# Performance work log

Measured on AMD Instinct MI355X. Metric: run time of the kernel, lower is better.

## Reference

```python
import jax, jax.numpy as jnp
import numpy as np

D_MODEL = 1024
N_HEAD = 16
D_HEAD = D_MODEL // N_HEAD
N_CTX = 2048
ROPE_BASE = 10000.0
SCALE = 1


def _rope_cache(seq_len, d_head, dtype=jnp.float32):
    inv_freq = 1.0 / (ROPE_BASE ** (jnp.arange(0, d_head, 2, dtype=jnp.float32) / d_head))
    t = jnp.arange(seq_len, dtype=jnp.float32)
    freqs = jnp.outer(t, inv_freq)              # [S, d_head/2]
    emb = jnp.concatenate([freqs, freqs], -1)   # [S, d_head]  (concat, per source)
    cos = jnp.cos(emb)[None, :, None, :].astype(dtype)
    sin = jnp.sin(emb)[None, :, None, :].astype(dtype)
    return cos, sin


def _apply_rope(x, cos, sin):
    # x: [B, S, H, Dh]; interleaved rotate (stack then flatten), per source
    x_even = x[..., 0::2]
    x_odd = x[..., 1::2]
    x_rot = jnp.stack([-x_odd, x_even], axis=-1).reshape(x.shape)
    return x * cos + x_rot * sin


def _rmsnorm(x, w):
    eps = jnp.finfo(x.dtype).eps  # torch RMSNorm default eps
    var = jnp.mean(jnp.square(x), axis=-1, keepdims=True)
    return x * jax.lax.rsqrt(var + eps) * w


def setup_inputs() -> dict:
    key = jax.random.key(0)
    ks = jax.random.split(key, 9)
    B, S = 2, N_CTX
    x = jax.random.normal(ks[0], (B, S, D_MODEL), jnp.float32)
    s = 0.02
    Wq = jax.random.normal(ks[1], (D_MODEL, D_MODEL), jnp.float32) * s
    bq = jax.random.normal(ks[2], (D_MODEL,), jnp.float32) * s
    Wk = jax.random.normal(ks[3], (D_MODEL, D_MODEL), jnp.float32) * s
    bk = jax.random.normal(ks[4], (D_MODEL,), jnp.float32) * s
    Wv = jax.random.normal(ks[5], (D_MODEL, D_MODEL), jnp.float32) * s
    bv = jax.random.normal(ks[6], (D_MODEL,), jnp.float32) * s
    Wo = jax.random.normal(ks[7], (D_MODEL, D_MODEL), jnp.float32) * s
    norm_w = jnp.ones((D_HEAD,), jnp.float32)
    return {"x": x, "Wq": Wq, "bq": bq, "Wk": Wk, "bk": bk,
            "Wv": Wv, "bv": bv, "Wo": Wo, "norm_w": norm_w}


def reference(x, Wq, bq, Wk, bk, Wv, bv, Wo, norm_w):
    B, S, _ = x.shape
    split = lambda t: t.reshape(B, S, N_HEAD, D_HEAD)
    q = split(x @ Wq.T + bq)
    k = split(x @ Wk.T + bk)
    v = split(x @ Wv.T + bv)
    cos, sin = _rope_cache(S, D_HEAD, x.dtype)
    q = _apply_rope(_rmsnorm(q, norm_w), cos, sin)
    k = _apply_rope(_rmsnorm(k, norm_w), cos, sin)
    scores = jnp.einsum('bqhd,bkhd->bhqk', q, k)
    causal = jnp.tril(jnp.ones((S, S), x.dtype))
    pattern = jnp.square(scores / D_HEAD) * causal  # quadratic score, masked
    z = jnp.einsum('bhqk,bkhd->bqhd', pattern, v).reshape(B, S, D_MODEL)
    return x + (z @ Wo.T) * SCALE
```

## Files before the change

### kernel.cpp

```cpp
#include <hip/hip_runtime.h>
#include <math.h>


typedef float  f32x4  __attribute__((ext_vector_type(4)));
typedef short  bf16x8 __attribute__((ext_vector_type(8)));
typedef float  vf4    __attribute__((ext_vector_type(4)));
typedef unsigned short u16x4 __attribute__((ext_vector_type(4)));

static __device__ __forceinline__ unsigned short f2bf(float f) {
    union { float f; unsigned int i; } c; c.f = f;
    unsigned int x = c.i;
    return (unsigned short)((x + 0x7fffu + ((x >> 16) & 1u)) >> 16);
}
static __device__ __forceinline__ f32x4 shfl_xor4(f32x4 v, int m) {
    f32x4 r;
    r[0] = __shfl_xor(v[0], m); r[1] = __shfl_xor(v[1], m);
    r[2] = __shfl_xor(v[2], m); r[3] = __shfl_xor(v[3], m);
    return r;
}
static __device__ __forceinline__ f32x4 rsq4(f32x4 v) {
    f32x4 r;
#pragma unroll
    for (int i = 0; i < 4; i++) r[i] = rsqrtf(v[i] * (1.0f / 64.0f) + 1.1920929e-07f);
    return r;
}
static __device__ __forceinline__ void cp16(const unsigned short* g, unsigned short* l) {
    __builtin_amdgcn_global_load_lds(
        (const __attribute__((address_space(1))) unsigned int*)g,
        (__attribute__((address_space(3))) unsigned int*)l, 16, 0, 0);
}

#define FOR_2(X)  X(0) X(1)
#define FOR_M(X)  X(0) X(1) X(2) X(3)
#define FOR_MN(X) X(0,0) X(0,1) X(0,2) X(0,3) X(1,0) X(1,1) X(1,2) X(1,3) \
                  X(2,0) X(2,1) X(2,2) X(2,3) X(3,0) X(3,1) X(3,2) X(3,3)
#define FOR_MN2(X) X(0,0) X(0,1) X(0,2) X(0,3) X(1,0) X(1,1) X(1,2) X(1,3)

#define MF(c,a,b) c = __builtin_amdgcn_mfma_f32_16x16x32_bf16(a, b, c, 0, 0, 0);

__global__ __launch_bounds__(256) void cvt_all(
    const float* __restrict__ x,  const float* __restrict__ Wq,
    const float* __restrict__ Wk, const float* __restrict__ Wv,
    const float* __restrict__ Wo,
    unsigned short* __restrict__ xb,  unsigned short* __restrict__ Wqb,
    unsigned short* __restrict__ Wkb, unsigned short* __restrict__ Wvb,
    unsigned short* __restrict__ Wob, int nx4, int nw4)
{
    int i = blockIdx.x * 256 + threadIdx.x;
    const float* s; unsigned short* d; int li;
    if (i < nx4) { s = x; d = xb; li = i; }
    else {
        int idx = i - nx4;
        int r = idx / nw4; li = idx - r * nw4;
        if (r >= 4) return;
        s = (r == 0) ? Wq : (r == 1) ? Wk : (r == 2) ? Wv : Wo;
        d = (r == 0) ? Wqb : (r == 1) ? Wkb : (r == 2) ? Wvb : Wob;
    }
    vf4 v = *(const vf4*)(s + (size_t)li * 4);
    u16x4 o;
#pragma unroll
    for (int j = 0; j < 4; j++) o[j] = f2bf(v[j]);
    *(u16x4*)(d + (size_t)li * 4) = o;
}

#define SS 136

__global__ __launch_bounds__(256, 3) void gemm_qkvz(
    const unsigned short* __restrict__ xb,
    const unsigned short* __restrict__ Wqb,
    const unsigned short* __restrict__ Wkb,
    const unsigned short* __restrict__ Wvb,
    const float* __restrict__ bqf, const float* __restrict__ bkf, const float* __restrict__ bvf,
    const float* __restrict__ nwp,
    unsigned short* __restrict__ qb, unsigned short* __restrict__ kb,
    unsigned short* __restrict__ vT)
{
    const int K = 1024;
    __shared__ unsigned short smem[24576];
    const int z = blockIdx.z;
    const unsigned short* Wb = (z == 0) ? Wqb : (z == 1) ? Wkb : Wvb;
    const float* bias = (z == 0) ? bqf : (z == 1) ? bkf : bvf;
    const int tid = threadIdx.x;
    const int n0 = blockIdx.x * 128;
    const int m0 = blockIdx.y * 128;
    const int lane = tid & 63, wid = tid >> 6;
    const int wy = wid >> 1, wx = wid & 1;
    const int l15 = lane & 15, quad = lane >> 4;
    const int r16 = lane >> 2;
    const int c8  = (lane & 3) * 8;

#define Z_DECL_ACC(mi,ni) f32x4 c##mi##ni = {0.f, 0.f, 0.f, 0.f};
    FOR_MN(Z_DECL_ACC)

#define Z_STAGE(BUF, KT) { \
        unsigned short* dstb = smem + (BUF) * 8192; \
        _Pragma("unroll") \
        for (int j = 0; j < 4; j++) { \
            const int ch = wid * 4 + j;           \
            const int mat = ch >> 3;              \
            const int row = (ch & 7) * 16 + r16; \
            const unsigned short* g = mat \
                ? Wb + (size_t)(n0 + row) * K + (KT) + c8 \
                : xb + (size_t)(m0 + row) * K + (KT) + c8; \
            cp16(g, &dstb[ch * 512]); \
        } }

#define Z_COMPUTE(BUF) { \
        const unsigned short* As_ = smem + (BUF) * 8192; \
        const unsigned short* Bs_ = As_ + 4096; \
        const bf16x8 a0 = *(const bf16x8*)&As_[(wy * 64 +  0 + l15) * 32 + quad * 8]; \
        const bf16x8 a1 = *(const bf16x8*)&As_[(wy * 64 + 16 + l15) * 32 + quad * 8]; \
        const bf16x8 a2 = *(const bf16x8*)&As_[(wy * 64 + 32 + l15) * 32 + quad * 8]; \
        const bf16x8 a3 = *(const bf16x8*)&As_[(wy * 64 + 48 + l15) * 32 + quad * 8]; \
        const bf16x8 b0 = *(const bf16x8*)&Bs_[(wx * 64 +  0 + l15) * 32 + quad * 8]; \
        const bf16x8 b1 = *(const bf16x8*)&Bs_[(wx * 64 + 16 + l15) * 32 + quad * 8]; \
        const bf16x8 b2 = *(const bf16x8*)&Bs_[(wx * 64 + 32 + l15) * 32 + quad * 8]; \
        const bf16x8 b3 = *(const bf16x8*)&Bs_[(wx * 64 + 48 + l15) * 32 + quad * 8]; \
        MF(c00,a0,b0) MF(c01,a0,b1) MF(c02,a0,b2) MF(c03,a0,b3) \
        MF(c10,a1,b0) MF(c11,a1,b1) MF(c12,a1,b2) MF(c13,a1,b3) \
        MF(c20,a2,b0) MF(c21,a2,b1) MF(c22,a2,b2) MF(c23,a2,b3) \
        MF(c30,a3,b0) MF(c31,a3,b1) MF(c32,a3,b2) MF(c33,a3,b3) }

    Z_STAGE(0, 0)
    Z_STAGE(1, 32)
    {
        int cbuf = 0, sbuf = 2;
        for (int it = 0; it < 31; ++it) {
            asm volatile("s_waitcnt vmcnt(4)" ::: "memory");
            __builtin_amdgcn_s_barrier();
            if (it < 30) { Z_STAGE(sbuf, (it + 2) * 32) }
            Z_COMPUTE(cbuf)
            asm volatile("s_waitcnt lgkmcnt(0)" ::: "memory");
            cbuf = (cbuf == 2) ? 0 : cbuf + 1;
            sbuf = (sbuf == 2) ? 0 : sbuf + 1;
        }
        asm volatile("s_waitcnt vmcnt(0)" ::: "memory");
        __builtin_amdgcn_s_barrier();
        Z_COMPUTE(cbuf)
    }
    __syncthreads();

    const float bs0 = bias[n0 + wx * 64 + l15];
    const float bs1 = bias[n0 + wx * 64 + 16 + l15];
    const float bs2 = bias[n0 + wx * 64 + 32 + l15];
    const float bs3 = bias[n0 + wx * 64 + 48 + l15];
#define Z_BIAS(mi) c##mi##0 += bs0; c##mi##1 += bs1; c##mi##2 += bs2; c##mi##3 += bs3;
    FOR_M(Z_BIAS)

    if (z < 2) {
        const float nww0 = nwp[l15],      nww1 = nwp[16 + l15];
        const float nww2 = nwp[32 + l15], nww3 = nwp[48 + l15];
        const float lf0 = expf(-(float)l15 * 0.28782313662425572f);
        const float lf1 = expf(-(float)(l15 + 16) * 0.28782313662425572f);

#define Z_S2(mi) f32x4 s2_##mi = c##mi##0*c##mi##0 + c##mi##1*c##mi##1 + \
                                 c##mi##2*c##mi##2 + c##mi##3*c##mi##3; \
        s2_##mi = s2_##mi + shfl_xor4(s2_##mi, 1); \
        s2_##mi = s2_##mi + shfl_xor4(s2_##mi, 2); \
        s2_##mi = s2_##mi + shfl_xor4(s2_##mi, 4); \
        s2_##mi = s2_##mi + shfl_xor4(s2_##mi, 8); \
        s2_##mi = rsq4(s2_##mi);
        FOR_M(Z_S2)

#define Z_ROPE_ONE(mi,ni,NW,CS,SN) { \
            float vn = c##mi##ni[r] * s2v[r] * NW; \
            float pt = __shfl_xor(vn, 1); \
            float rot = (lane & 1) ? pt : -pt; \
            smem[mrow * SS + wx * 64 + (ni) * 16 + l15] = f2bf((vn * (CS) + rot * (SN)) * 0.125f); }
#define Z_ROPE_MI(mi) { f32x4 s2v = s2_##mi; \
            _Pragma("unroll") \
            for (int r = 0; r < 4; r++) { \
                const int mrow = wy * 64 + (mi) * 16 + quad * 4 + r; \
                const float t = (float)((m0 + mrow) & 2047); \
                const float a0 = t * lf0, a1 = t * lf1; \
                const float cs0 = cosf(a0), sn0 = sinf(a0); \
                const float cs1 = cosf(a1), sn1 = sinf(a1); \
                Z_ROPE_ONE(mi,0,nww0,cs0,sn0) Z_ROPE_ONE(mi,1,nww1,cs1,sn1) \
                Z_ROPE_ONE(mi,2,nww2,cs0,sn0) Z_ROPE_ONE(mi,3,nww3,cs1,sn1) } }
        FOR_M(Z_ROPE_MI)

        __syncthreads();
        unsigned short* dst = z ? kb : qb;
#pragma unroll
        for (int it = 0; it < 8; it++) {
            const int linear = tid + it * 256;
            const int row = linear >> 4, cb = linear & 15;
            *(bf16x8*)(dst + (size_t)(m0 + row) * 1024 + n0 + cb * 8) =
                *(const bf16x8*)&smem[row * SS + cb * 8];
        }
    } else {
#define Z_VST(mi,ni) { _Pragma("unroll") \
            for (int r = 0; r < 4; r++) { \
                const int mrow = wy * 64 + (mi) * 16 + quad * 4 + r; \
                smem[(wx * 64 + (ni) * 16 + l15) * SS + mrow] = f2bf(c##mi##ni[r]); } }
        FOR_MN(Z_VST)
        __syncthreads();
        const int b = m0 >> 11, tok0 = m0 & 2047;
#pragma unroll
        for (int it = 0; it < 8; it++) {
            const int linear = tid + it * 256;
            const int rowd = linear >> 4, cb = linear & 15;
            const int head_g = (n0 >> 6) + (rowd >> 6);
            const int d = rowd & 63;
            *(bf16x8*)(vT + (((size_t)b * 16 + head_g) * 64 + d) * 2048 + tok0 + cb * 8) =
                *(const bf16x8*)&smem[rowd * SS + cb * 8];
        }
    }
}

__global__ __launch_bounds__(512) void gemm_out(
    const unsigned short* __restrict__ zb,
    const unsigned short* __restrict__ Wob,
    const float* __restrict__ x, float* __restrict__ out, int M)
{
    const int K = 1024;
    __shared__ unsigned short smem[24576];
    const int tid = threadIdx.x;
    const int n0 = blockIdx.x * 128;
    const int m0 = blockIdx.y * 128;
    const int lane = tid & 63, wid = tid >> 6;
    const int wy = wid >> 1, wx = wid & 1;
    const int l15 = lane & 15, quad = lane >> 4;
    const int r16 = lane >> 2;
    const int c8  = (lane & 3) * 8;

#define G_DECL_ACC(mi,ni) f32x4 c##mi##ni = {0.f, 0.f, 0.f, 0.f};
    FOR_MN2(G_DECL_ACC)

#define O_STAGE(BUF, KT) { \
        unsigned short* dstb = smem + (BUF) * 8192; \
        _Pragma("unroll") \
        for (int j = 0; j < 2; j++) { \
            const int ch = wid * 2 + j;           \
            const int mat = ch >> 3;              \
            const int row = (ch & 7) * 16 + r16; \
            const unsigned short* g = (mat == 0) \
                ? zb  + (size_t)(m0 + row) * K + (KT) + c8 \
                : Wob + (size_t)(n0 + row) * K + (KT) + c8; \
            cp16(g, &dstb[ch * 512]); \
        } }

#define O_COMPUTE(BUF) { \
        const unsigned short* As_ = smem + (BUF) * 8192; \
        const unsigned short* Ws_ = As_ + 4096; \
        const bf16x8 a0 = *(const bf16x8*)&As_[(wy * 32 +  0 + l15) * 32 + quad * 8]; \
        const bf16x8 a1 = *(const bf16x8*)&As_[(wy * 32 + 16 + l15) * 32 + quad * 8]; \
        const bf16x8 b0 = *(const bf16x8*)&Ws_[(wx * 64 +  0 + l15) * 32 + quad * 8]; \
        const bf16x8 b1 = *(const bf16x8*)&Ws_[(wx * 64 + 16 + l15) * 32 + quad * 8]; \
        const bf16x8 b2 = *(const bf16x8*)&Ws_[(wx * 64 + 32 + l15) * 32 + quad * 8]; \
        const bf16x8 b3 = *(const bf16x8*)&Ws_[(wx * 64 + 48 + l15) * 32 + quad * 8]; \
        MF(c00,a0,b0) MF(c01,a0,b1) MF(c02,a0,b2) MF(c03,a0,b3) \
        MF(c10,a1,b0) MF(c11,a1,b1) MF(c12,a1,b2) MF(c13,a1,b3) }

    O_STAGE(0, 0)
    O_STAGE(1, 32)
    {
        int cbuf = 0, sbuf = 2;
        for (int it = 0; it < 31; ++it) {
            asm volatile("s_waitcnt vmcnt(2)" ::: "memory");
            __builtin_amdgcn_s_barrier();
            if (it < 30) { O_STAGE(sbuf, (it + 2) * 32) }
            O_COMPUTE(cbuf)
            asm volatile("s_waitcnt lgkmcnt(0)" ::: "memory");
            cbuf = (cbuf == 2) ? 0 : cbuf + 1;
            sbuf = (sbuf == 2) ? 0 : sbuf + 1;
        }
        asm volatile("s_waitcnt vmcnt(0)" ::: "memory");
        __builtin_amdgcn_s_barrier();
        O_COMPUTE(cbuf)
    }

#define G_OUTST(mi,ni) { _Pragma("unroll") \
        for (int r = 0; r < 4; r++) { \
            const int m = m0 + wy * 32 + (mi) * 16 + quad * 4 + r; \
            const int n = n0 + wx * 64 + (ni) * 16 + l15; \
            out[(size_t)m * 1024 + n] = c##mi##ni[r] + x[(size_t)m * 1024 + n]; } }
    FOR_MN2(G_OUTST)
}

__global__ __launch_bounds__(256) void attn_mfma(
    const unsigned short* __restrict__ qb, const unsigned short* __restrict__ kb,
    const unsigned short* __restrict__ vT, unsigned short* __restrict__ zb)
{
    __shared__ unsigned short Qs[128 * 72];
    __shared__ unsigned short Ks[64 * 72];
    __shared__ unsigned short Vs[64 * 72];
    __shared__ unsigned short Pm[128 * 72];
    const int tid = threadIdx.x;

    const int bid = blockIdx.x;
    const int halfsz = gridDim.x >> 1;
    const int half = (bid >= halfsz) ? 1 : 0;
    const int r = bid - half * halfsz;
    const int qt = half ? (r & 7) : 15 - (r & 7);
    const int bh = r >> 3;

    const int b = bh >> 4, h = bh & 15;
    const int lane = tid & 63, wq = tid >> 6;
    const int l15 = lane & 15, quad = lane >> 4;
    const size_t tokbase = (size_t)b * 2048;
    const int q0 = qt * 128;

#pragma unroll
    for (int j = 0; j < 4; j++) {
        const int u = tid + j * 256;
        const int row = u >> 3, seg = (u & 7) * 8;
        bf16x8 v = *(const bf16x8*)(qb + (tokbase + q0 + row) * 1024 + h * 64 + seg);
        *(bf16x8*)&Qs[row * 72 + seg] = v;
    }
    __syncthreads();
    const bf16x8 aq00 = *(const bf16x8*)&Qs[(wq * 32 + l15) * 72 + quad * 8];
    const bf16x8 aq01 = *(const bf16x8*)&Qs[(wq * 32 + l15) * 72 + 32 + quad * 8];
    const bf16x8 aq10 = *(const bf16x8*)&Qs[(wq * 32 + 16 + l15) * 72 + quad * 8];
    const bf16x8 aq11 = *(const bf16x8*)&Qs[(wq * 32 + 16 + l15) * 72 + 32 + quad * 8];

    const int kr = tid >> 3;
    const int sg = (tid & 7) * 8;

    bf16x8 pk0, pk1, pv0, pv1;
#define A_GLB(KT) { \
        pk0 = *(const bf16x8*)(kb + (tokbase + (KT) * 64 + kr) * 1024 + h * 64 + sg); \
        pk1 = *(const bf16x8*)(kb + (tokbase + (KT) * 64 + kr + 32) * 1024 + h * 64 + sg); \
        pv0 = *(const bf16x8*)(vT + ((size_t)bh * 64 + kr) * 2048 + (KT) * 64 + sg); \
        pv1 = *(const bf16x8*)(vT + ((size_t)bh * 64 + kr + 32) * 2048 + (KT) * 64 + sg); }

#define A_DECL_Z(mi,n) f32x4 z_##mi##n = {0.f, 0.f, 0.f, 0.f};
    FOR_MN2(A_DECL_Z)

    const int nkt = 2 * qt + 2;
    A_GLB(0)
    for (int kt = 0; kt < nkt; kt++) {
        __syncthreads();
        *(bf16x8*)&Ks[kr * 72 + sg] = pk0;
        *(bf16x8*)&Ks[(kr + 32) * 72 + sg] = pk1;
        *(bf16x8*)&Vs[kr * 72 + sg] = pv0;
        *(bf16x8*)&Vs[(kr + 32) * 72 + sg] = pv1;
        __syncthreads();
        if (kt + 1 < nkt) A_GLB(kt + 1)

#define A_DECL_S(mi,n) f32x4 s_##mi##n = {0.f, 0.f, 0.f, 0.f};
        FOR_MN2(A_DECL_S)
#define A_QKH(KS, AQ0, AQ1) { \
        bf16x8 b0 = *(const bf16x8*)&Ks[(l15) * 72 + (KS) * 32 + quad * 8]; \
        bf16x8 b1 = *(const bf16x8*)&Ks[(16 + l15) * 72 + (KS) * 32 + quad * 8]; \
        bf16x8 b2 = *(const bf16x8*)&Ks[(32 + l15) * 72 + (KS) * 32 + quad * 8]; \
        bf16x8 b3 = *(const bf16x8*)&Ks[(48 + l15) * 72 + (KS) * 32 + quad * 8]; \
        s_00 = __builtin_amdgcn_mfma_f32_16x16x32_bf16(AQ0, b0, s_00, 0, 0, 0); \
        s_01 = __builtin_amdgcn_mfma_f32_16x16x32_bf16(AQ0, b1, s_01, 0, 0, 0); \
        s_02 = __builtin_amdgcn_mfma_f32_16x16x32_bf16(AQ0, b2, s_02, 0, 0, 0); \
        s_03 = __builtin_amdgcn_mfma_f32_16x16x32_bf16(AQ0, b3, s_03, 0, 0, 0); \
        s_10 = __builtin_amdgcn_mfma_f32_16x16x32_bf16(AQ1, b0, s_10, 0, 0, 0); \
        s_11 = __builtin_amdgcn_mfma_f32_16x16x32_bf16(AQ1, b1, s_11, 0, 0, 0); \
        s_12 = __builtin_amdgcn_mfma_f32_16x16x32_bf16(AQ1, b2, s_12, 0, 0, 0); \
        s_13 = __builtin_amdgcn_mfma_f32_16x16x32_bf16(AQ1, b3, s_13, 0, 0, 0); }
        A_QKH(0, aq00, aq10)
        A_QKH(1, aq01, aq11)

        const bool needmask = (kt >= 2 * qt);
#define A_PSTORE(mi,n) { \
        f32x4 p4 = s_##mi##n * s_##mi##n; \
        if (needmask) { _Pragma("unroll") \
            for (int r2 = 0; r2 < 4; r2++) \
                if (kt * 64 + (n) * 16 + l15 > q0 + wq * 32 + (mi) * 16 + quad * 4 + r2) p4[r2] = 0.f; } \
        _Pragma("unroll") \
        for (int r2 = 0; r2 < 4; r2++) \
            Pm[(wq * 32 + (mi) * 16 + quad * 4 + r2) * 72 + (n) * 16 + l15] = f2bf(p4[r2]); }
        FOR_MN2(A_PSTORE)

#define A_PVH(KS) { \
        bf16x8 ap0 = *(const bf16x8*)&Pm[(wq * 32 + l15) * 72 + (KS) * 32 + quad * 8]; \
        bf16x8 ap1 = *(const bf16x8*)&Pm[(wq * 32 + 16 + l15) * 72 + (KS) * 32 + quad * 8]; \
        bf16x8 u0 = *(const bf16x8*)&Vs[(l15) * 72 + (KS) * 32 + quad * 8]; \
        bf16x8 u1 = *(const bf16x8*)&Vs[(16 + l15) * 72 + (KS) * 32 + quad * 8]; \
        bf16x8 u2 = *(const bf16x8*)&Vs[(32 + l15) * 72 + (KS) * 32 + quad * 8]; \
        bf16x8 u3 = *(const bf16x8*)&Vs[(48 + l15) * 72 + (KS) * 32 + quad * 8]; \
        z_00 = __builtin_amdgcn_mfma_f32_16x16x32_bf16(ap0, u0, z_00, 0, 0, 0); \
        z_01 = __builtin_amdgcn_mfma_f32_16x16x32_bf16(ap0, u1, z_01, 0, 0, 0); \
        z_02 = __builtin_amdgcn_mfma_f32_16x16x32_bf16(ap0, u2, z_02, 0, 0, 0); \
        z_03 = __builtin_amdgcn_mfma_f32_16x16x32_bf16(ap0, u3, z_03, 0, 0, 0); \
        z_10 = __builtin_amdgcn_mfma_f32_16x16x32_bf16(ap1, u0, z_10, 0, 0, 0); \
        z_11 = __builtin_amdgcn_mfma_f32_16x16x32_bf16(ap1, u1, z_11, 0, 0, 0); \
        z_12 = __builtin_amdgcn_mfma_f32_16x16x32_bf16(ap1, u2, z_12, 0, 0, 0); \
        z_13 = __builtin_amdgcn_mfma_f32_16x16x32_bf16(ap1, u3, z_13, 0, 0, 0); }
        A_PVH(0)
        A_PVH(1)
    }

#define A_ZST(mi,n) { _Pragma("unroll") \
        for (int r2 = 0; r2 < 4; r2++) \
            Pm[(wq * 32 + (mi) * 16 + quad * 4 + r2) * 72 + (n) * 16 + l15] = f2bf(z_##mi##n[r2]); }
    FOR_MN2(A_ZST)
#pragma unroll
    for (int it = 0; it < 4; it++) {
        const int linear = it * 64 + lane;
        const int row = linear >> 3, cb = linear & 7;
        *(bf16x8*)(zb + (tokbase + q0 + wq * 32 + row) * 1024 + h * 64 + cb * 8) =
            *(const bf16x8*)&Pm[(wq * 32 + row) * 72 + cb * 8];
    }
}

extern "C" void kernel_launch(void* const* d_in, const int* in_sizes, int n_in,
                              void* d_out, int out_size, void* d_ws, size_t ws_size,
                              hipStream_t stream)
{
    const float* x  = (const float*)d_in[0];
    const float* Wq = (const float*)d_in[1];
    const float* bq = (const float*)d_in[2];
    const float* Wk = (const float*)d_in[3];
    const float* bk = (const float*)d_in[4];
    const float* Wv = (const float*)d_in[5];
    const float* bv = (const float*)d_in[6];
    const float* Wo = (const float*)d_in[7];
    const float* nw = (const float*)d_in[8];
    float* out = (float*)d_out;

    const int D = 1024;
    const int M = in_sizes[0] / D;

    unsigned short* xbb = (unsigned short*)d_ws;
    unsigned short* Wqb = xbb + (size_t)M * D;
    unsigned short* Wkb = Wqb + (size_t)D * D;
    unsigned short* Wvb = Wkb + (size_t)D * D;
    unsigned short* Wob = Wvb + (size_t)D * D;
    unsigned short* qbw = Wob + (size_t)D * D;
    unsigned short* kbw = qbw + (size_t)M * D;
    unsigned short* vTw = kbw + (size_t)M * D;
    unsigned short* zbw = vTw + (size_t)M * D;

    const int nx4 = M * D / 4, nw4 = D * D / 4;
    const int ncvt = nx4 + 4 * nw4;
    cvt_all<<<(ncvt + 255) / 256, 256, 0, stream>>>(
        x, Wq, Wk, Wv, Wo, xbb, Wqb, Wkb, Wvb, Wob, nx4, nw4);

    gemm_qkvz<<<dim3(D / 128, M / 128, 3), 256, 0, stream>>>(
        xbb, Wqb, Wkb, Wvb, bq, bk, bv, nw, qbw, kbw, vTw);

    attn_mfma<<<dim3((M / 2048) * 16 * 16), 256, 0, stream>>>(qbw, kbw, vTw, zbw);

    gemm_out<<<dim3(D / 128, M / 128), 512, 0, stream>>>(zbw, Wob, x, out, M);
}
```

Baseline: 197.2 us.

## Enlarge QKV GEMM tile to 256x256 with XOR-swizzled LDS and BK=64

Restructures the fused QKV projection GEMM to use 256x256 output tiles per 512-thread block with 8 waves, each computing a 128x64 sub-tile. K-step grows to 64 with an XOR-swizzled LDS layout to avoid bank conflicts, and the pipeline becomes double-buffered. Epilogue staging through shared memory is split into two halves to fit the buffer. The aim is more data reuse per global load and fewer blocks, at the cost of fewer blocks (96) than CUs, more registers and 128KB of LDS per block.

```diff
diff --git a/kernel.cpp b/kernel.cpp
--- a/kernel.cpp
+++ b/kernel.cpp
@@ -30,11 +30,13 @@
         (__attribute__((address_space(3))) unsigned int*)l, 16, 0, 0);
 }
 
-#define FOR_2(X)  X(0) X(1)
 #define FOR_M(X)  X(0) X(1) X(2) X(3)
-#define FOR_MN(X) X(0,0) X(0,1) X(0,2) X(0,3) X(1,0) X(1,1) X(1,2) X(1,3) \
-                  X(2,0) X(2,1) X(2,2) X(2,3) X(3,0) X(3,1) X(3,2) X(3,3)
+#define FOR_M8(X) X(0) X(1) X(2) X(3) X(4) X(5) X(6) X(7)
 #define FOR_MN2(X) X(0,0) X(0,1) X(0,2) X(0,3) X(1,0) X(1,1) X(1,2) X(1,3)
+#define FOR_MN84(X) X(0,0) X(0,1) X(0,2) X(0,3) X(1,0) X(1,1) X(1,2) X(1,3) \
+                    X(2,0) X(2,1) X(2,2) X(2,3) X(3,0) X(3,1) X(3,2) X(3,3) \
+                    X(4,0) X(4,1) X(4,2) X(4,3) X(5,0) X(5,1) X(5,2) X(5,3) \
+                    X(6,0) X(6,1) X(6,2) X(6,3) X(7,0) X(7,1) X(7,2) X(7,3)
 
 #define MF(c,a,b) c = __builtin_amdgcn_mfma_f32_16x16x32_bf16(a, b, c, 0, 0, 0);
 
@@ -63,9 +65,9 @@
     *(u16x4*)(d + (size_t)li * 4) = o;
 }
 
-#define SS 136
-
-__global__ __launch_bounds__(256, 3) void gemm_qkvz(
+#define SS2 264
+
+__global__ __launch_bounds__(512, 2) void gemm_qkvz(
     const unsigned short* __restrict__ xb,
     const unsigned short* __restrict__ Wqb,
     const unsigned short* __restrict__ Wkb,
@@ -76,68 +78,73 @@
     unsigned short* __restrict__ vT)
 {
     const int K = 1024;
-    __shared__ unsigned short smem[24576];
+    __shared__ unsigned short smem[65536];
     const int z = blockIdx.z;
     const unsigned short* Wb = (z == 0) ? Wqb : (z == 1) ? Wkb : Wvb;
     const float* bias = (z == 0) ? bqf : (z == 1) ? bkf : bvf;
     const int tid = threadIdx.x;
-    const int n0 = blockIdx.x * 128;
-    const int m0 = blockIdx.y * 128;
+    const int n0 = blockIdx.x * 256;
+    const int m0 = blockIdx.y * 256;
     const int lane = tid & 63, wid = tid >> 6;
-    const int wy = wid >> 1, wx = wid & 1;
+    const int wy = wid >> 2, wx = wid & 3;
     const int l15 = lane & 15, quad = lane >> 4;
-    const int r16 = lane >> 2;
-    const int c8  = (lane & 3) * 8;
+    const int sw = (l15 & 7) << 4;
+    const int srow = tid >> 3;
+    const int sc16 = tid & 7;
 
 #define Z_DECL_ACC(mi,ni) f32x4 c##mi##ni = {0.f, 0.f, 0.f, 0.f};
-    FOR_MN(Z_DECL_ACC)
-
-#define Z_STAGE(BUF, KT) { \
-        unsigned short* dstb = smem + (BUF) * 8192; \
+    FOR_MN84(Z_DECL_ACC)
+
+#define ZSTAGE(BUF, KT) { \
+        unsigned short* dstb = smem + (BUF) * 32768; \
         _Pragma("unroll") \
         for (int j = 0; j < 4; j++) { \
-            const int ch = wid * 4 + j;           \
-            const int mat = ch >> 3;              \
-            const int row = (ch & 7) * 16 + r16; \
-            const unsigned short* g = mat \
-                ? Wb + (size_t)(n0 + row) * K + (KT) + c8 \
-                : xb + (size_t)(m0 + row) * K + (KT) + c8; \
-            cp16(g, &dstb[ch * 512]); \
+            const int row = j * 64 + srow; \
+            const int gc = sc16 ^ (row & 7); \
+            cp16(xb + (size_t)(m0 + row) * K + (KT) + gc * 8, \
+                 dstb + row * 64 + sc16 * 8); \
+            cp16(Wb + (size_t)(n0 + row) * K + (KT) + gc * 8, \
+                 dstb + 16384 + row * 64 + sc16 * 8); \
         } }
 
-#define Z_COMPUTE(BUF) { \
-        const unsigned short* As_ = smem + (BUF) * 8192; \
-        const unsigned short* Bs_ = As_ + 4096; \
-        const bf16x8 a0 = *(const bf16x8*)&As_[(wy * 64 +  0 + l15) * 32 + quad * 8]; \
-        const bf16x8 a1 = *(const bf16x8*)&As_[(wy * 64 + 16 + l15) * 32 + quad * 8]; \
-        const bf16x8 a2 = *(const bf16x8*)&As_[(wy * 64 + 32 + l15) * 32 + quad * 8]; \
-        const bf16x8 a3 = *(const bf16x8*)&As_[(wy * 64 + 48 + l15) * 32 + quad * 8]; \
-        const bf16x8 b0 = *(const bf16x8*)&Bs_[(wx * 64 +  0 + l15) * 32 + quad * 8]; \
-        const bf16x8 b1 = *(const bf16x8*)&Bs_[(wx * 64 + 16 + l15) * 32 + quad * 8]; \
-        const bf16x8 b2 = *(const bf16x8*)&Bs_[(wx * 64 + 32 + l15) * 32 + quad * 8]; \
-        const bf16x8 b3 = *(const bf16x8*)&Bs_[(wx * 64 + 48 + l15) * 32 + quad * 8]; \
-        MF(c00,a0,b0) MF(c01,a0,b1) MF(c02,a0,b2) MF(c03,a0,b3) \
-        MF(c10,a1,b0) MF(c11,a1,b1) MF(c12,a1,b2) MF(c13,a1,b3) \
-        MF(c20,a2,b0) MF(c21,a2,b1) MF(c22,a2,b2) MF(c23,a2,b3) \
-        MF(c30,a3,b0) MF(c31,a3,b1) MF(c32,a3,b2) MF(c33,a3,b3) }
-
-    Z_STAGE(0, 0)
-    Z_STAGE(1, 32)
-    {
-        int cbuf = 0, sbuf = 2;
-        for (int it = 0; it < 31; ++it) {
-            asm volatile("s_waitcnt vmcnt(4)" ::: "memory");
-            __builtin_amdgcn_s_barrier();
-            if (it < 30) { Z_STAGE(sbuf, (it + 2) * 32) }
-            Z_COMPUTE(cbuf)
-            asm volatile("s_waitcnt lgkmcnt(0)" ::: "memory");
-            cbuf = (cbuf == 2) ? 0 : cbuf + 1;
-            sbuf = (sbuf == 2) ? 0 : sbuf + 1;
-        }
-        asm volatile("s_waitcnt vmcnt(0)" ::: "memory");
-        __builtin_amdgcn_s_barrier();
-        Z_COMPUTE(cbuf)
-    }
+#define ZA_DECL(mi) const bf16x8 a##mi = *(const bf16x8*)&As_[(wy * 128 + (mi) * 16 + l15) * 64 + offk];
+#define ZB_DECL(ni) const bf16x8 b##ni = *(const bf16x8*)&Bs_[(wx * 64 + (ni) * 16 + l15) * 64 + offk];
+#define ZMF_ROW(mi) MF(c##mi##0, a##mi, b0) MF(c##mi##1, a##mi, b1) \
+                    MF(c##mi##2, a##mi, b2) MF(c##mi##3, a##mi, b3)
+
+#define ZCOMPUTE(BUF) { \
+        const unsigned short* As_ = smem + (BUF) * 32768; \
+        const unsigned short* Bs_ = As_ + 16384; \
+        _Pragma("unroll") \
+        for (int ks = 0; ks < 2; ks++) { \
+            const int offk = ((ks * 64 + quad * 16) ^ sw) >> 1; \
+            FOR_M8(ZA_DECL) \
+            ZB_DECL(0) ZB_DECL(1) ZB_DECL(2) ZB_DECL(3) \
+            FOR_M8(ZMF_ROW) \
+        } }
+
+#define VM8 asm volatile("s_waitcnt vmcnt(8)" ::: "memory");
+#define VM0 asm volatile("s_waitcnt vmcnt(0)" ::: "memory");
+#define LG0 asm volatile("s_waitcnt lgkmcnt(0)" ::: "memory");
+#define BAR __builtin_amdgcn_s_barrier();
+
+    ZSTAGE(0, 0)
+    for (int p = 0; p < 7; ++p) {
+        ZSTAGE(1, (2 * p + 1) * 64)
+        VM8 BAR
+        ZCOMPUTE(0)
+        LG0 BAR
+        ZSTAGE(0, (2 * p + 2) * 64)
+        VM8 BAR
+        ZCOMPUTE(1)
+        LG0 BAR
+    }
+    ZSTAGE(1, 15 * 64)
+    VM8 BAR
+    ZCOMPUTE(0)
+    LG0 BAR
+    VM0 BAR
+    ZCOMPUTE(1)
     __syncthreads();
 
     const float bs0 = bias[n0 + wx * 64 + l15];
@@ -145,7 +152,7 @@
     const float bs2 = bias[n0 + wx * 64 + 32 + l15];
     const float bs3 = bias[n0 + wx * 64 + 48 + l15];
 #define Z_BIAS(mi) c##mi##0 += bs0; c##mi##1 += bs1; c##mi##2 += bs2; c##mi##3 += bs3;
-    FOR_M(Z_BIAS)
+    FOR_M8(Z_BIAS)
 
     if (z < 2) {
         const float nww0 = nwp[l15],      nww1 = nwp[16 + l15];
@@ -160,50 +167,60 @@
         s2_##mi = s2_##mi + shfl_xor4(s2_##mi, 4); \
         s2_##mi = s2_##mi + shfl_xor4(s2_##mi, 8); \
         s2_##mi = rsq4(s2_##mi);
-        FOR_M(Z_S2)
+        FOR_M8(Z_S2)
+
+        unsigned short* dst = z ? kb : qb;
 
 #define Z_ROPE_ONE(mi,ni,NW,CS,SN) { \
             float vn = c##mi##ni[r] * s2v[r] * NW; \
             float pt = __shfl_xor(vn, 1); \
             float rot = (lane & 1) ? pt : -pt; \
-            smem[mrow * SS + wx * 64 + (ni) * 16 + l15] = f2bf((vn * (CS) + rot * (SN)) * 0.125f); }
+            smem[sr * SS2 + wx * 64 + (ni) * 16 + l15] = f2bf((vn * (CS) + rot * (SN)) * 0.125f); }
 #define Z_ROPE_MI(mi) { f32x4 s2v = s2_##mi; \
             _Pragma("unroll") \
             for (int r = 0; r < 4; r++) { \
-                const int mrow = wy * 64 + (mi) * 16 + quad * 4 + r; \
-                const float t = (float)((m0 + mrow) & 2047); \
+                const int sr = (mi) * 16 + quad * 4 + r; \
+                const float t = (float)((m0 + wy * 128 + sr) & 2047); \
                 const float a0 = t * lf0, a1 = t * lf1; \
                 const float cs0 = cosf(a0), sn0 = sinf(a0); \
                 const float cs1 = cosf(a1), sn1 = sinf(a1); \
                 Z_ROPE_ONE(mi,0,nww0,cs0,sn0) Z_ROPE_ONE(mi,1,nww1,cs1,sn1) \
                 Z_ROPE_ONE(mi,2,nww2,cs0,sn0) Z_ROPE_ONE(mi,3,nww3,cs1,sn1) } }
-        FOR_M(Z_ROPE_MI)
-
-        __syncthreads();
-        unsigned short* dst = z ? kb : qb;
-#pragma unroll
-        for (int it = 0; it < 8; it++) {
-            const int linear = tid + it * 256;
-            const int row = linear >> 4, cb = linear & 15;
-            *(bf16x8*)(dst + (size_t)(m0 + row) * 1024 + n0 + cb * 8) =
-                *(const bf16x8*)&smem[row * SS + cb * 8];
+
+#pragma unroll
+        for (int h2 = 0; h2 < 2; h2++) {
+            if (wy == h2) { FOR_M8(Z_ROPE_MI) }
+            __syncthreads();
+#pragma unroll
+            for (int it = 0; it < 8; it++) {
+                const int linear = tid + it * 512;
+                const int row = linear >> 5, cb = linear & 31;
+                *(bf16x8*)(dst + (size_t)(m0 + h2 * 128 + row) * 1024 + n0 + cb * 8) =
+                    *(const bf16x8*)&smem[row * SS2 + cb * 8];
+            }
+            __syncthreads();
         }
     } else {
+        const int b = m0 >> 11, tok0 = m0 & 2047;
 #define Z_VST(mi,ni) { _Pragma("unroll") \
             for (int r = 0; r < 4; r++) { \
-                const int mrow = wy * 64 + (mi) * 16 + quad * 4 + r; \
-                smem[(wx * 64 + (ni) * 16 + l15) * SS + mrow] = f2bf(c##mi##ni[r]); } }
-        FOR_MN(Z_VST)
-        __syncthreads();
-        const int b = m0 >> 11, tok0 = m0 & 2047;
-#pragma unroll
-        for (int it = 0; it < 8; it++) {
-            const int linear = tid + it * 256;
-            const int rowd = linear >> 4, cb = linear & 15;
-            const int head_g = (n0 >> 6) + (rowd >> 6);
-            const int d = rowd & 63;
-            *(bf16x8*)(vT + (((size_t)b * 16 + head_g) * 64 + d) * 2048 + tok0 + cb * 8) =
-                *(const bf16x8*)&smem[rowd * SS + cb * 8];
+                const int mrow = wy * 128 + (mi) * 16 + quad * 4 + r; \
+                smem[((wx & 1) * 64 + (ni) * 16 + l15) * SS2 + mrow] = f2bf(c##mi##ni[r]); } }
+#pragma unroll
+        for (int c2 = 0; c2 < 2; c2++) {
+            if ((wx >> 1) == c2) { FOR_MN84(Z_VST) }
+            __syncthreads();
+#pragma unroll
+            for (int it = 0; it < 8; it++) {
+                const int linear = tid + it * 512;
+                const int rowd = linear >> 5, cb = linear & 31;
+                const int ncol = c2 * 128 + rowd;
+                const int head_g = (n0 >> 6) + (ncol >> 6);
+                const int d = ncol & 63;
+                *(bf16x8*)(vT + (((size_t)b * 16 + head_g) * 64 + d) * 2048 + tok0 + cb * 8) =
+                    *(const bf16x8*)&smem[rowd * SS2 + cb * 8];
+            }
+            __syncthreads();
         }
     }
 }
@@ -231,8 +248,8 @@
         unsigned short* dstb = smem + (BUF) * 8192; \
         _Pragma("unroll") \
         for (int j = 0; j < 2; j++) { \
-            const int ch = wid * 2 + j;           \
-            const int mat = ch >> 3;              \
+            const int ch = wid * 2 + j; \
+            const int mat = ch >> 3; \
             const int row = (ch & 7) * 16 + r16; \
             const unsigned short* g = (mat == 0) \
                 ? zb  + (size_t)(m0 + row) * K + (KT) + c8 \
@@ -432,7 +449,7 @@
     cvt_all<<<(ncvt + 255) / 256, 256, 0, stream>>>(
         x, Wq, Wk, Wv, Wo, xbb, Wqb, Wkb, Wvb, Wob, nx4, nw4);
 
-    gemm_qkvz<<<dim3(D / 128, M / 128, 3), 256, 0, stream>>>(
+    gemm_qkvz<<<dim3(D / 256, M / 256, 3), 512, 0, stream>>>(
         xbb, Wqb, Wkb, Wvb, bq, bk, bv, nw, qbw, kbw, vTw);
 
     attn_mfma<<<dim3((M / 2048) * 16 * 16), 256, 0, stream>>>(qbw, kbw, vTw, zbw);
```

Measured after the change: 405.1 us. 105% more time.

## Use 4-wave 64x64 warp tiles in output GEMM and raise MFMA priority in attention

Applied to the files above, without the earlier changes.

The output projection GEMM drops from 8 waves to 4 per block. Each wave now computes a 64x64 sub-tile with 16 accumulators, which improves register-level reuse of the LDS fragments. Each thread issues twice as many async copies per stage, and the vmcnt wait is adjusted to match. Separately, the attention kernel wraps its QK and PV MFMA blocks in s_setprio so that matrix work is scheduled ahead of other waves' memory or ALU work. The trade-off is higher register pressure and fewer waves for latency hiding in the GEMM.

```diff
diff --git a/kernel.cpp b/kernel.cpp
--- a/kernel.cpp
+++ b/kernel.cpp
@@ -30,7 +30,6 @@
         (__attribute__((address_space(3))) unsigned int*)l, 16, 0, 0);
 }
 
-#define FOR_2(X)  X(0) X(1)
 #define FOR_M(X)  X(0) X(1) X(2) X(3)
 #define FOR_MN(X) X(0,0) X(0,1) X(0,2) X(0,3) X(1,0) X(1,1) X(1,2) X(1,3) \
                   X(2,0) X(2,1) X(2,2) X(2,3) X(3,0) X(3,1) X(3,2) X(3,3)
@@ -208,7 +207,7 @@
     }
 }
 
-__global__ __launch_bounds__(512) void gemm_out(
+__global__ __launch_bounds__(256, 3) void gemm_out(
     const unsigned short* __restrict__ zb,
     const unsigned short* __restrict__ Wob,
     const float* __restrict__ x, float* __restrict__ out, int M)
@@ -225,39 +224,43 @@
     const int c8  = (lane & 3) * 8;
 
 #define G_DECL_ACC(mi,ni) f32x4 c##mi##ni = {0.f, 0.f, 0.f, 0.f};
-    FOR_MN2(G_DECL_ACC)
+    FOR_MN(G_DECL_ACC)
 
 #define O_STAGE(BUF, KT) { \
         unsigned short* dstb = smem + (BUF) * 8192; \
         _Pragma("unroll") \
-        for (int j = 0; j < 2; j++) { \
-            const int ch = wid * 2 + j;           \
+        for (int j = 0; j < 4; j++) { \
+            const int ch = wid * 4 + j;           \
             const int mat = ch >> 3;              \
             const int row = (ch & 7) * 16 + r16; \
-            const unsigned short* g = (mat == 0) \
-                ? zb  + (size_t)(m0 + row) * K + (KT) + c8 \
-                : Wob + (size_t)(n0 + row) * K + (KT) + c8; \
+            const unsigned short* g = mat \
+                ? Wob + (size_t)(n0 + row) * K + (KT) + c8 \
+                : zb  + (size_t)(m0 + row) * K + (KT) + c8; \
             cp16(g, &dstb[ch * 512]); \
         } }
 
 #define O_COMPUTE(BUF) { \
         const unsigned short* As_ = smem + (BUF) * 8192; \
-        const unsigned short* Ws_ = As_ + 4096; \
-        const bf16x8 a0 = *(const bf16x8*)&As_[(wy * 32 +  0 + l15) * 32 + quad * 8]; \
-        const bf16x8 a1 = *(const bf16x8*)&As_[(wy * 32 + 16 + l15) * 32 + quad * 8]; \
-        const bf16x8 b0 = *(const bf16x8*)&Ws_[(wx * 64 +  0 + l15) * 32 + quad * 8]; \
-        const bf16x8 b1 = *(const bf16x8*)&Ws_[(wx * 64 + 16 + l15) * 32 + quad * 8]; \
-        const bf16x8 b2 = *(const bf16x8*)&Ws_[(wx * 64 + 32 + l15) * 32 + quad * 8]; \
-        const bf16x8 b3 = *(const bf16x8*)&Ws_[(wx * 64 + 48 + l15) * 32 + quad * 8]; \
+        const unsigned short* Bs_ = As_ + 4096; \
+        const bf16x8 a0 = *(const bf16x8*)&As_[(wy * 64 +  0 + l15) * 32 + quad * 8]; \
+        const bf16x8 a1 = *(const bf16x8*)&As_[(wy * 64 + 16 + l15) * 32 + quad * 8]; \
+        const bf16x8 a2 = *(const bf16x8*)&As_[(wy * 64 + 32 + l15) * 32 + quad * 8]; \
+        const bf16x8 a3 = *(const bf16x8*)&As_[(wy * 64 + 48 + l15) * 32 + quad * 8]; \
+        const bf16x8 b0 = *(const bf16x8*)&Bs_[(wx * 64 +  0 + l15) * 32 + quad * 8]; \
+        const bf16x8 b1 = *(const bf16x8*)&Bs_[(wx * 64 + 16 + l15) * 32 + quad * 8]; \
+        const bf16x8 b2 = *(const bf16x8*)&Bs_[(wx * 64 + 32 + l15) * 32 + quad * 8]; \
+        const bf16x8 b3 = *(const bf16x8*)&Bs_[(wx * 64 + 48 + l15) * 32 + quad * 8]; \
         MF(c00,a0,b0) MF(c01,a0,b1) MF(c02,a0,b2) MF(c03,a0,b3) \
-        MF(c10,a1,b0) MF(c11,a1,b1) MF(c12,a1,b2) MF(c13,a1,b3) }
+        MF(c10,a1,b0) MF(c11,a1,b1) MF(c12,a1,b2) MF(c13,a1,b3) \
+        MF(c20,a2,b0) MF(c21,a2,b1) MF(c22,a2,b2) MF(c23,a2,b3) \
+        MF(c30,a3,b0) MF(c31,a3,b1) MF(c32,a3,b2) MF(c33,a3,b3) }
 
     O_STAGE(0, 0)
     O_STAGE(1, 32)
     {
         int cbuf = 0, sbuf = 2;
         for (int it = 0; it < 31; ++it) {
-            asm volatile("s_waitcnt vmcnt(2)" ::: "memory");
+            asm volatile("s_waitcnt vmcnt(4)" ::: "memory");
             __builtin_amdgcn_s_barrier();
             if (it < 30) { O_STAGE(sbuf, (it + 2) * 32) }
             O_COMPUTE(cbuf)
@@ -272,10 +275,10 @@
 
 #define G_OUTST(mi,ni) { _Pragma("unroll") \
         for (int r = 0; r < 4; r++) { \
-            const int m = m0 + wy * 32 + (mi) * 16 + quad * 4 + r; \
+            const int m = m0 + wy * 64 + (mi) * 16 + quad * 4 + r; \
             const int n = n0 + wx * 64 + (ni) * 16 + l15; \
             out[(size_t)m * 1024 + n] = c##mi##ni[r] + x[(size_t)m * 1024 + n]; } }
-    FOR_MN2(G_OUTST)
+    FOR_MN(G_OUTST)
 }
 
 __global__ __launch_bounds__(256) void attn_mfma(
@@ -353,8 +356,10 @@
         s_11 = __builtin_amdgcn_mfma_f32_16x16x32_bf16(AQ1, b1, s_11, 0, 0, 0); \
         s_12 = __builtin_amdgcn_mfma_f32_16x16x32_bf16(AQ1, b2, s_12, 0, 0, 0); \
         s_13 = __builtin_amdgcn_mfma_f32_16x16x32_bf16(AQ1, b3, s_13, 0, 0, 0); }
+        __builtin_amdgcn_s_setprio(1);
         A_QKH(0, aq00, aq10)
         A_QKH(1, aq01, aq11)
+        __builtin_amdgcn_s_setprio(0);
 
         const bool needmask = (kt >= 2 * qt);
 #define A_PSTORE(mi,n) { \
@@ -382,8 +387,10 @@
         z_11 = __builtin_amdgcn_mfma_f32_16x16x32_bf16(ap1, u1, z_11, 0, 0, 0); \
         z_12 = __builtin_amdgcn_mfma_f32_16x16x32_bf16(ap1, u2, z_12, 0, 0, 0); \
         z_13 = __builtin_amdgcn_mfma_f32_16x16x32_bf16(ap1, u3, z_13, 0, 0, 0); }
+        __builtin_amdgcn_s_setprio(1);
         A_PVH(0)
         A_PVH(1)
+        __builtin_amdgcn_s_setprio(0);
     }
 
 #define A_ZST(mi,n) { _Pragma("unroll") \
@@ -437,5 +444,5 @@
 
     attn_mfma<<<dim3((M / 2048) * 16 * 16), 256, 0, stream>>>(qbw, kbw, vTw, zbw);
 
-    gemm_out<<<dim3(D / 128, M / 128), 512, 0, stream>>>(zbw, Wob, x, out, M);
-}
+    gemm_out<<<dim3(D / 128, M / 128), 256, 0, stream>>>(zbw, Wob, x, out, M);
+}
```

Result: no change. 196.9 us (-0.2%).
